# Kernel tuning notes

Hardware: AMD Instinct MI355X
Metric: run time of the kernel (lower is better)

Reference implementation:

```python
import jax, jax.numpy as jnp
import numpy as np

N_NODES = 100_000
N_EDGES_RAND = 800_000
N_GRAPHS = 2048
IN_FEATS = 74        # CanonicalAtomFeaturizer size
HEADS = 4            # dgllife GAT default num_heads
OUT_FEATS = 32       # dgllife GAT default hidden_feats=[32,32]
PRED_DIM = 128
NEG_SLOPE = 0.2      # dgllife default alpha


def setup_inputs() -> dict:
    key = jax.random.key(0)
    ks = jax.random.split(key, 16)
    feats = jax.random.normal(ks[0], (N_NODES, IN_FEATS), jnp.float32)
    src_r = jax.random.randint(ks[1], (N_EDGES_RAND,), 0, N_NODES, dtype=jnp.int32)
    dst_r = jax.random.randint(ks[2], (N_EDGES_RAND,), 0, N_NODES, dtype=jnp.int32)
    loops = jnp.arange(N_NODES, dtype=jnp.int32)  # self-loops -> no zero in-degree
    src = jnp.concatenate([src_r, loops])
    dst = jnp.concatenate([dst_r, loops])
    # sorted, every graph non-empty, ~49 nodes per molecule
    graph_ids = ((jnp.arange(N_NODES, dtype=jnp.int64) * N_GRAPHS) // N_NODES).astype(jnp.int32)

    def lin(k, i, o):
        return (jax.random.normal(k, (i, o), jnp.float32) / np.sqrt(i)).astype(jnp.float32)

    HF = HEADS * OUT_FEATS
    return {
        'feats': feats, 'src': src, 'dst': dst, 'graph_ids': graph_ids,
        'fc1_w': lin(ks[3], IN_FEATS, HF),
        'attn_l1': jax.random.normal(ks[4], (HEADS, OUT_FEATS), jnp.float32) * 0.1,
        'attn_r1': jax.random.normal(ks[5], (HEADS, OUT_FEATS), jnp.float32) * 0.1,
        'res1_w': lin(ks[6], IN_FEATS, HF),   # residual proj (in != heads*out)
        'bias1': jnp.zeros((HF,), jnp.float32),
        'fc2_w': lin(ks[7], HF, HF),
        'attn_l2': jax.random.normal(ks[8], (HEADS, OUT_FEATS), jnp.float32) * 0.1,
        'attn_r2': jax.random.normal(ks[9], (HEADS, OUT_FEATS), jnp.float32) * 0.1,
        'bias2': jnp.zeros((HF,), jnp.float32),
        'ww': lin(ks[10], OUT_FEATS, 1),
        'wb': jnp.zeros((1,), jnp.float32),
        'tw': lin(ks[11], 2 * OUT_FEATS, PRED_DIM),
        'tb': jnp.zeros((PRED_DIM,), jnp.float32),
    }


def _gat_conv(h, src, dst, fc_w, attn_l, attn_r, bias, res):
    # h: (N, Din) -> (N, H, F). Faithful to dgl.nn.GATConv (bias=True, residual=True).
    N = h.shape[0]
    feat = (h @ fc_w).reshape(N, HEADS, OUT_FEATS)          # (N,H,F)
    el = jnp.sum(feat * attn_l, axis=-1)                    # (N,H)
    er = jnp.sum(feat * attn_r, axis=-1)                    # (N,H)
    e = jax.nn.leaky_relu(el[src] + er[dst], NEG_SLOPE)     # (E,H)
    # edge softmax over incoming edges of each dst node (numerically stable)
    emax = jax.ops.segment_max(e, dst, num_segments=N)      # (N,H)
    ee = jnp.exp(e - emax[dst])
    denom = jax.ops.segment_sum(ee, dst, num_segments=N)    # (N,H)
    a = ee / denom[dst]                                     # (E,H)
    rst = jax.ops.segment_sum(a[:, :, None] * feat[src], dst, num_segments=N)  # (N,H,F)
    return rst + res + bias.reshape(1, HEADS, OUT_FEATS)


def reference(feats, src, dst, graph_ids, fc1_w, attn_l1, attn_r1, res1_w, bias1,
              fc2_w, attn_l2, attn_r2, bias2, ww, wb, tw, tb):
    N = feats.shape[0]
    # Layer 1: residual needs projection (74 != 128); agg 'flatten' + ELU
    res1 = (feats @ res1_w).reshape(N, HEADS, OUT_FEATS)
    h1 = _gat_conv(feats, src, dst, fc1_w, attn_l1, attn_r1, bias1, res1)
    h1 = jax.nn.elu(h1.reshape(N, HEADS * OUT_FEATS))
    # Layer 2: identity residual (128 == heads*out); agg 'mean', no activation
    res2 = h1.reshape(N, HEADS, OUT_FEATS)
    h2 = _gat_conv(h1, src, dst, fc2_w, attn_l2, attn_r2, bias2, res2)
    node_feats = jnp.mean(h2, axis=1)                       # (N, 32)
    # WeightedSumAndMax readout
    w = jax.nn.sigmoid(node_feats @ ww + wb)                # (N,1)
    h_sum = jax.ops.segment_sum(w * node_feats, graph_ids, num_segments=N_GRAPHS)
    h_max = jax.ops.segment_max(node_feats, graph_ids, num_segments=N_GRAPHS)
    g = jnp.concatenate([h_sum, h_max], axis=-1)            # (B, 64)
    return g @ tw + tb                                      # (B, PRED_DIM)
```

## Files before the change

kernel.cpp:

```cpp
#include <hip/hip_runtime.h>
#include <hip/hip_bf16.h>


#define HEADS 4
#define OUTF 32
#define HF 128
#define IN_FEATS 74
#define PRED_DIM 128
#define NEG_SLOPE 0.2f
#define NEG_INF_ENC 0x007fffffu
#define LOG2E 1.4426950408889634f
#define KP1 48
#define KP2 64

typedef __hip_bfloat16 bf16;
typedef __hip_bfloat162 bf16x2;
typedef __attribute__((ext_vector_type(8))) short bf16x8v;
typedef __attribute__((ext_vector_type(4))) float f32x4v;
typedef __attribute__((ext_vector_type(2))) float f32x2v;

__device__ __forceinline__ unsigned enc_f(float f) {
  unsigned u = __float_as_uint(f);
  return (u & 0x80000000u) ? ~u : (u | 0x80000000u);
}
__device__ __forceinline__ float dec_f(unsigned k) {
  return (k & 0x80000000u) ? __uint_as_float(k & 0x7fffffffu)
                           : __uint_as_float(~k);
}
__device__ __forceinline__ unsigned pack_bf16(float a, float b) {
  bf16x2 h = __float22bfloat162_rn(make_float2(a, b));
  return *(unsigned*)&h;
}
__device__ __forceinline__ float2 unpack_bf16(unsigned u) {
  bf16x2 h = *(bf16x2*)&u;
  return __bfloat1622float2(h);
}
__device__ __forceinline__ float lrelu(float v) {
  return fmaxf(v, NEG_SLOPE * v);
}

__global__ __launch_bounds__(256) void prep_w(
    const float* __restrict__ W1, const float* __restrict__ W2,
    const float* __restrict__ W3, unsigned* __restrict__ WT1,
    unsigned* __restrict__ WT2, unsigned* __restrict__ WT3,
    int* __restrict__ deg, int N) {
  int t = blockIdx.x * 256 + threadIdx.x;
  if (t < N) deg[t] = 0;
  if (t < 128 * KP1) {
    int c = t / KP1, kp = t % KP1;
    int k = kp * 2;
    float a1 = (k < IN_FEATS) ? W1[k * HF + c] : 0.f;
    float b1 = (k + 1 < IN_FEATS) ? W1[(k + 1) * HF + c] : 0.f;
    float a2 = (k < IN_FEATS) ? W2[k * HF + c] : 0.f;
    float b2 = (k + 1 < IN_FEATS) ? W2[(k + 1) * HF + c] : 0.f;
    WT1[t] = pack_bf16(a1, b1);
    WT2[t] = pack_bf16(a2, b2);
  } else {
    int u = t - 128 * KP1;
    if (u < 128 * KP2) {
      int c = u / KP2, kp = u % KP2;
      int k = kp * 2;
      WT3[u] = pack_bf16(W3[k * HF + c], W3[(k + 1) * HF + c]);
    }
  }
}


template <int K>
__device__ __forceinline__ bf16x8v load_a_f32(const float* __restrict__ X,
                                              int row, int N, int ks, int q) {
  unsigned v[4] = {0u, 0u, 0u, 0u};
  if (row < N) {
    const float* base = X + (size_t)row * K;
    int k = ks * 32 + q * 8;
#pragma unroll
    for (int j = 0; j < 4; ++j) {
      int kk = k + j * 2;
      if (kk + 1 < K) {
        float2 f = *(const float2*)&base[kk];
        v[j] = pack_bf16(f.x, f.y);
      } else if (kk < K) {
        v[j] = pack_bf16(base[kk], 0.f);
      }
    }
  }
  union { unsigned u[4]; bf16x8v v8; } r;
  r.u[0] = v[0]; r.u[1] = v[1]; r.u[2] = v[2]; r.u[3] = v[3];
  return r.v8;
}

__device__ __forceinline__ void scores_epilogue(
    const f32x4v* acc, const float* __restrict__ attn_l,
    const float* __restrict__ attn_r, float* __restrict__ el,
    float* __restrict__ er, int n0, int w, int q, int cc, int N) {
#pragma unroll
  for (int r = 0; r < 4; ++r) {
    int n = n0 + w * 16 + q * 4 + r;
    float pls[4], prs[4];
#pragma unroll
    for (int h = 0; h < 4; ++h) {
      float pl = acc[2 * h][r] * attn_l[h * 32 + cc] +
                 acc[2 * h + 1][r] * attn_l[h * 32 + 16 + cc];
      float pr = acc[2 * h][r] * attn_r[h * 32 + cc] +
                 acc[2 * h + 1][r] * attn_r[h * 32 + 16 + cc];
#pragma unroll
      for (int off = 1; off < 16; off <<= 1) {
        pl += __shfl_xor(pl, off);
        pr += __shfl_xor(pr, off);
      }
      pls[h] = pl;
      prs[h] = pr;
    }
    if (cc == 0 && n < N) {
#pragma unroll
      for (int h = 0; h < 4; ++h) {
        el[n * HEADS + h] = pls[h] * LOG2E;
        er[n * HEADS + h] = prs[h] * LOG2E;
      }
    }
  }
}

template <int K, int KP>
__global__ __launch_bounds__(256) void mfma_gemm(
    const bf16* __restrict__ X, const unsigned* __restrict__ WT,
    const float* __restrict__ attn_l, const float* __restrict__ attn_r,
    bf16* __restrict__ out, float* __restrict__ el, float* __restrict__ er,
    int N) {
  const int tid = threadIdx.x;
  const int w = tid >> 6;
  const int lane = tid & 63;
  const int cc = lane & 15;
  const int q = lane >> 4;
  const int n0 = blockIdx.x * 64;
  const int arow = n0 + w * 16 + cc;

  f32x4v acc[8];
#pragma unroll
  for (int t = 0; t < 8; ++t) acc[t] = f32x4v{0.f, 0.f, 0.f, 0.f};

  constexpr int KSTEPS = (K + 31) / 32;
#pragma unroll
  for (int ks = 0; ks < KSTEPS; ++ks) {
    bf16x8v a = *(const bf16x8v*)&X[(size_t)arow * K + ks * 32 + q * 8];
#pragma unroll
    for (int t = 0; t < 8; ++t) {
      bf16x8v b = *(const bf16x8v*)&WT[(t * 16 + cc) * KP + ks * 16 + q * 4];
      acc[t] = __builtin_amdgcn_mfma_f32_16x16x32_bf16(a, b, acc[t], 0, 0, 0);
    }
  }
#pragma unroll
  for (int r = 0; r < 4; ++r) {
    int n = n0 + w * 16 + q * 4 + r;
    if (n < N) {
#pragma unroll
      for (int t = 0; t < 8; ++t)
        out[(size_t)n * HF + t * 16 + cc] = __float2bfloat16(acc[t][r]);
    }
  }
  scores_epilogue(acc, attn_l, attn_r, el, er, n0, w, q, cc, N);
}

template <int K, int KP>
__global__ __launch_bounds__(256) void mfma_dual(
    const float* __restrict__ X, const unsigned* __restrict__ WT1,
    const unsigned* __restrict__ WT2, const float* __restrict__ attn_l,
    const float* __restrict__ attn_r, bf16* __restrict__ outA,
    bf16* __restrict__ outB, float* __restrict__ el, float* __restrict__ er,
    int N) {
  const int tid = threadIdx.x;
  const int w = tid >> 6;
  const int lane = tid & 63;
  const int cc = lane & 15;
  const int q = lane >> 4;
  const int n0 = blockIdx.x * 64;
  const int arow = n0 + w * 16 + cc;

  f32x4v acc1[8], acc2[8];
#pragma unroll
  for (int t = 0; t < 8; ++t) {
    acc1[t] = f32x4v{0.f, 0.f, 0.f, 0.f};
    acc2[t] = f32x4v{0.f, 0.f, 0.f, 0.f};
  }

  constexpr int KSTEPS = (K + 31) / 32;
#pragma unroll
  for (int ks = 0; ks < KSTEPS; ++ks) {
    bf16x8v a = load_a_f32<K>(X, arow, N, ks, q);
#pragma unroll
    for (int t = 0; t < 8; ++t) {
      bf16x8v b1 = *(const bf16x8v*)&WT1[(t * 16 + cc) * KP + ks * 16 + q * 4];
      bf16x8v b2 = *(const bf16x8v*)&WT2[(t * 16 + cc) * KP + ks * 16 + q * 4];
      acc1[t] = __builtin_amdgcn_mfma_f32_16x16x32_bf16(a, b1, acc1[t], 0, 0, 0);
      acc2[t] = __builtin_amdgcn_mfma_f32_16x16x32_bf16(a, b2, acc2[t], 0, 0, 0);
    }
  }
#pragma unroll
  for (int r = 0; r < 4; ++r) {
    int n = n0 + w * 16 + q * 4 + r;
    if (n < N) {
#pragma unroll
      for (int t = 0; t < 8; ++t) {
        outA[(size_t)n * HF + t * 16 + cc] = __float2bfloat16(acc1[t][r]);
        outB[(size_t)n * HF + t * 16 + cc] = __float2bfloat16(acc2[t][r]);
      }
    }
  }
  scores_epilogue(acc1, attn_l, attn_r, el, er, n0, w, q, cc, N);
}

__global__ __launch_bounds__(256) void hist_kernel(
    const int* __restrict__ dst, int* __restrict__ deg,
    int* __restrict__ rank, float* __restrict__ hsum,
    unsigned* __restrict__ hmax, int E, int g32) {
  int e = blockIdx.x * 256 + threadIdx.x;
  if (e < g32) {
    hsum[e] = 0.f;
    hmax[e] = NEG_INF_ENC;
  }
  if (e < E) rank[e] = atomicAdd(&deg[dst[e]], 1);
}

__global__ __launch_bounds__(256) void scan1_kernel(
    const int* __restrict__ deg, int* __restrict__ row_ptr,
    int* __restrict__ bsum, int N) {
  const int base = blockIdx.x * 2048;
  const int tbase = base + threadIdx.x * 8;
  int vals[8];
  int tsum = 0;
#pragma unroll
  for (int i = 0; i < 8; ++i) {
    int idx = tbase + i;
    vals[i] = (idx < N) ? deg[idx] : 0;
    tsum += vals[i];
  }
  const int lane = threadIdx.x & 63, wv = threadIdx.x >> 6;
  int incl = tsum;
#pragma unroll
  for (int off = 1; off < 64; off <<= 1) {
    int nv = __shfl_up(incl, off);
    if (lane >= off) incl += nv;
  }
  __shared__ int wsum[4];
  if (lane == 63) wsum[wv] = incl;
  __syncthreads();
  int woff = 0;
  for (int w = 0; w < wv; ++w) woff += wsum[w];
  int run = woff + incl - tsum;
#pragma unroll
  for (int i = 0; i < 8; ++i) {
    int idx = tbase + i;
    if (idx < N) row_ptr[idx] = run;
    run += vals[i];
  }
  if (threadIdx.x == 255) bsum[blockIdx.x] = woff + incl;
}

__global__ __launch_bounds__(64) void scan2_kernel(
    const int* __restrict__ bsum, int* __restrict__ bpre, int NB) {
  const int lane = threadIdx.x;
  int running = 0;
  for (int c = 0; c < NB; c += 64) {
    int v = (c + lane < NB) ? bsum[c + lane] : 0;
    int incl = v;
#pragma unroll
    for (int off = 1; off < 64; off <<= 1) {
      int nv = __shfl_up(incl, off);
      if (lane >= off) incl += nv;
    }
    if (c + lane < NB) bpre[c + lane] = running + incl - v;
    running += __shfl(incl, 63);
  }
}

__global__ __launch_bounds__(256) void scan3_kernel(
    int* __restrict__ row_ptr, const int* __restrict__ bpre, int N, int E) {
  int t = blockIdx.x * 256 + threadIdx.x;
  if (t < N) row_ptr[t] += bpre[t >> 11];
  if (t == 0) row_ptr[N] = E;
}

__global__ __launch_bounds__(256) void scatter_kernel(
    const int* __restrict__ src, const int* __restrict__ dst,
    const int* __restrict__ row_ptr, const int* __restrict__ rank,
    int* __restrict__ ssorted, int E) {
  int e = blockIdx.x * 256 + threadIdx.x;
  if (e >= E) return;
  if (e < 16) ssorted[E + e] = 0;
  int d = dst[e];
  ssorted[row_ptr[d] + rank[e]] = src[e];
}


#define E8_LOAD(i, e_)                                                      \
  const int s##i = __builtin_amdgcn_readfirstlane(ssorted[e_]);             \
  const float xl##i = el[(unsigned)s##i * HEADS + h];                       \
  const unsigned fu##i = *(const unsigned*)&feat[(unsigned)s##i * HF + c2];
#define E8_CALC(i)                                                          \
  {                                                                         \
    float xx = __builtin_amdgcn_exp2f(lrelu(xl##i + ern));                  \
    f32x2v ff;                                                              \
    ff.x = __uint_as_float(fu##i << 16);                                    \
    ff.y = __uint_as_float(fu##i & 0xffff0000u);                            \
    ssum += xx;                                                             \
    axy = __builtin_elementwise_fma(f32x2v{xx, xx}, ff, axy);               \
  }
#define E8_CALC_PRED(i, e_)                                                 \
  {                                                                         \
    float xx = __builtin_amdgcn_exp2f(lrelu(xl##i + ern));                  \
    xx = ((e_) + i < re) ? xx : 0.f;                                        \
    f32x2v ff;                                                              \
    ff.x = __uint_as_float(fu##i << 16);                                    \
    ff.y = __uint_as_float(fu##i & 0xffff0000u);                            \
    ssum += xx;                                                             \
    axy = __builtin_elementwise_fma(f32x2v{xx, xx}, ff, axy);               \
  }

#define AGG_LOOP                                                            \
  f32x2v axy = {0.f, 0.f};                                                  \
  float ssum = 0.f;                                                         \
  const int dg = re - rb;                                                   \
  if (dg <= 8) {                                                            \
    E8_LOAD(0, rb) E8_LOAD(1, rb + 1) E8_LOAD(2, rb + 2)                    \
    E8_LOAD(3, rb + 3) E8_LOAD(4, rb + 4) E8_LOAD(5, rb + 5)                \
    E8_LOAD(6, rb + 6) E8_LOAD(7, rb + 7)                                   \
    E8_CALC_PRED(0, rb) E8_CALC_PRED(1, rb) E8_CALC_PRED(2, rb)             \
    E8_CALC_PRED(3, rb) E8_CALC_PRED(4, rb) E8_CALC_PRED(5, rb)             \
    E8_CALC_PRED(6, rb) E8_CALC_PRED(7, rb)                                 \
  } else if (dg <= 16) {                                                    \
    E8_LOAD(0, rb) E8_LOAD(1, rb + 1) E8_LOAD(2, rb + 2)                    \
    E8_LOAD(3, rb + 3) E8_LOAD(4, rb + 4) E8_LOAD(5, rb + 5)                \
    E8_LOAD(6, rb + 6) E8_LOAD(7, rb + 7)                                   \
    E8_LOAD(8, rb + 8) E8_LOAD(9, rb + 9) E8_LOAD(10, rb + 10)              \
    E8_LOAD(11, rb + 11) E8_LOAD(12, rb + 12) E8_LOAD(13, rb + 13)          \
    E8_LOAD(14, rb + 14) E8_LOAD(15, rb + 15)                               \
    E8_CALC(0) E8_CALC(1) E8_CALC(2) E8_CALC(3)                             \
    E8_CALC(4) E8_CALC(5) E8_CALC(6) E8_CALC(7)                             \
    E8_CALC_PRED(8, rb) E8_CALC_PRED(9, rb) E8_CALC_PRED(10, rb)            \
    E8_CALC_PRED(11, rb) E8_CALC_PRED(12, rb) E8_CALC_PRED(13, rb)          \
    E8_CALC_PRED(14, rb) E8_CALC_PRED(15, rb)                               \
  } else {                                                                  \
    int e = rb;                                                             \
    for (; e + 8 <= re; e += 8) {                                           \
      E8_LOAD(0, e) E8_LOAD(1, e + 1) E8_LOAD(2, e + 2) E8_LOAD(3, e + 3)   \
      E8_LOAD(4, e + 4) E8_LOAD(5, e + 5) E8_LOAD(6, e + 6)                 \
      E8_LOAD(7, e + 7)                                                     \
      E8_CALC(0) E8_CALC(1) E8_CALC(2) E8_CALC(3)                           \
      E8_CALC(4) E8_CALC(5) E8_CALC(6) E8_CALC(7)                           \
    }                                                                       \
    if (e < re) {                                                           \
      E8_LOAD(0, e) E8_LOAD(1, e + 1) E8_LOAD(2, e + 2) E8_LOAD(3, e + 3)   \
      E8_LOAD(4, e + 4) E8_LOAD(5, e + 5) E8_LOAD(6, e + 6)                 \
      E8_LOAD(7, e + 7)                                                     \
      E8_CALC_PRED(0, e) E8_CALC_PRED(1, e) E8_CALC_PRED(2, e)              \
      E8_CALC_PRED(3, e) E8_CALC_PRED(4, e) E8_CALC_PRED(5, e)              \
      E8_CALC_PRED(6, e) E8_CALC_PRED(7, e)                                 \
    }                                                                       \
  }                                                                         \
  float ax = axy.x, ay = axy.y;

__global__ __launch_bounds__(256) void agg1_fused(
    const int* __restrict__ row_ptr, const int* __restrict__ ssorted,
    const float* __restrict__ el, const float* __restrict__ er,
    const bf16* __restrict__ feat, const bf16* __restrict__ res,
    bf16* __restrict__ H, const float* __restrict__ bias, int N) {
  int n = blockIdx.x * 4 + (threadIdx.x >> 6);
  if (n >= N) return;
  const int lane = threadIdx.x & 63;
  const int c2 = lane * 2, h = lane >> 4;
  const int rb = __builtin_amdgcn_readfirstlane(row_ptr[n]);
  const int re = __builtin_amdgcn_readfirstlane(row_ptr[n + 1]);
  const float ern = er[(unsigned)n * HEADS + h];

  AGG_LOOP

  float inv = 1.f / ssum;
  float2 r = unpack_bf16(*(const unsigned*)&res[(unsigned)n * HF + c2]);
  float2 bi = *(const float2*)&bias[c2];
  float vx = fmaf(ax, inv, r.x + bi.x);
  float vy = fmaf(ay, inv, r.y + bi.y);
  vx = (vx > 0.f) ? vx : expm1f(vx);
  vy = (vy > 0.f) ? vy : expm1f(vy);
  *(unsigned*)&H[(unsigned)n * HF + c2] = pack_bf16(vx, vy);
}

__global__ __launch_bounds__(256) void agg2_fused(
    const int* __restrict__ row_ptr, const int* __restrict__ ssorted,
    const float* __restrict__ el, const float* __restrict__ er,
    const bf16* __restrict__ feat, const bf16* __restrict__ h1,
    const float* __restrict__ bias, const float* __restrict__ ww,
    const float* __restrict__ wb, const int* __restrict__ gids,
    float* __restrict__ hsum, unsigned* __restrict__ hmax, int N) {
  int n = blockIdx.x * 4 + (threadIdx.x >> 6);
  if (n >= N) return;
  const int lane = threadIdx.x & 63;
  const int c2 = lane * 2, h = lane >> 4;
  const int rb = __builtin_amdgcn_readfirstlane(row_ptr[n]);
  const int re = __builtin_amdgcn_readfirstlane(row_ptr[n + 1]);
  const float ern = er[(unsigned)n * HEADS + h];

  AGG_LOOP

  float inv = 1.f / ssum;
  float2 r = unpack_bf16(*(const unsigned*)&h1[(unsigned)n * HF + c2]);
  float2 bi = *(const float2*)&bias[c2];
  ax = fmaf(ax, inv, r.x + bi.x);
  ay = fmaf(ay, inv, r.y + bi.y);
#pragma unroll
  for (int off = 16; off < 64; off <<= 1) {
    ax += __shfl_xor(ax, off);
    ay += __shfl_xor(ay, off);
  }
  ax *= 0.25f;
  ay *= 0.25f;
  int c = c2 & 31;
  float d = fmaf(ax, ww[c], ay * ww[c + 1]);
#pragma unroll
  for (int off = 1; off < 16; off <<= 1) d += __shfl_xor(d, off);
  float wv = 1.f / (1.f + __expf(-(d + wb[0])));
  if (lane < 16) {
    int g = gids[n];
    atomicAdd(&hsum[g * OUTF + c], wv * ax);
    atomicAdd(&hsum[g * OUTF + c + 1], wv * ay);
    atomicMax(&hmax[g * OUTF + c], enc_f(ax));
    atomicMax(&hmax[g * OUTF + c + 1], enc_f(ay));
  }
}

__global__ __launch_bounds__(256) void final_gemm_kernel(
    const float* __restrict__ hsum, const unsigned* __restrict__ hmax,
    const float* __restrict__ tw, const float* __restrict__ tb,
    float* __restrict__ out, int G) {
  __shared__ float tws[64 * PRED_DIM];
  for (int i = threadIdx.x; i < 64 * PRED_DIM; i += 256) tws[i] = tw[i];
  __syncthreads();
  int g = blockIdx.x * 2 + (threadIdx.x >> 7);
  int p = threadIdx.x & 127;
  if (g >= G) return;
  float acc = tb[p];
#pragma unroll
  for (int k = 0; k < OUTF; ++k)
    acc = fmaf(hsum[g * OUTF + k], tws[k * PRED_DIM + p], acc);
#pragma unroll
  for (int k = 0; k < OUTF; ++k)
    acc = fmaf(dec_f(hmax[g * OUTF + k]), tws[(OUTF + k) * PRED_DIM + p], acc);
  out[(size_t)g * PRED_DIM + p] = acc;
}

static inline int cdiv(long long a, int b) { return (int)((a + b - 1) / b); }

extern "C" void kernel_launch(void* const* d_in, const int* in_sizes, int n_in,
                              void* d_out, int out_size, void* d_ws,
                              size_t ws_size, hipStream_t stream) {
  const float* feats   = (const float*)d_in[0];
  const int*   src     = (const int*)d_in[1];
  const int*   dst     = (const int*)d_in[2];
  const int*   gids    = (const int*)d_in[3];
  const float* fc1_w   = (const float*)d_in[4];
  const float* attn_l1 = (const float*)d_in[5];
  const float* attn_r1 = (const float*)d_in[6];
  const float* res1_w  = (const float*)d_in[7];
  const float* bias1   = (const float*)d_in[8];
  const float* fc2_w   = (const float*)d_in[9];
  const float* attn_l2 = (const float*)d_in[10];
  const float* attn_r2 = (const float*)d_in[11];
  const float* bias2   = (const float*)d_in[12];
  const float* ww      = (const float*)d_in[13];
  const float* wb      = (const float*)d_in[14];
  const float* tw      = (const float*)d_in[15];
  const float* tb      = (const float*)d_in[16];
  float* out = (float*)d_out;

  const int N = in_sizes[0] / IN_FEATS;
  const int E = in_sizes[1];
  const int G = out_size / PRED_DIM;
  const int NB = cdiv(N, 2048);

  bf16* A = (bf16*)d_ws;
  bf16* B = A + (size_t)N * HF;
  bf16* H = B + (size_t)N * HF;
  float* el = (float*)(H + (size_t)N * HF);
  float* er = el + (size_t)N * HEADS;
  float* hsum = er + (size_t)N * HEADS;
  unsigned* hmax = (unsigned*)(hsum + (size_t)G * OUTF);
  int* deg     = (int*)(hmax + (size_t)G * OUTF);
  int* row_ptr = deg + N;
  int* ssorted = row_ptr + (N + 1);
  int* rank    = ssorted + E + 16;
  int* bsum    = rank + E;
  int* bpre    = bsum + NB;
  unsigned* WT1 = (unsigned*)(((uintptr_t)(bpre + NB) + 15) &
                              ~(uintptr_t)15);
  unsigned* WT2 = WT1 + 128 * KP1;
  unsigned* WT3 = WT2 + 128 * KP1;

  const int gblk = cdiv(N, 64);
  const int nwblk = cdiv(N, 4);

  prep_w<<<cdiv(N, 256), 256, 0, stream>>>(fc1_w, res1_w, fc2_w, WT1, WT2,
                                           WT3, deg, N);
  hist_kernel<<<cdiv(E, 256), 256, 0, stream>>>(dst, deg, rank, hsum, hmax, E,
                                                G * OUTF);
  scan1_kernel<<<NB, 256, 0, stream>>>(deg, row_ptr, bsum, N);
  scan2_kernel<<<1, 64, 0, stream>>>(bsum, bpre, NB);
  scan3_kernel<<<cdiv(N, 256), 256, 0, stream>>>(row_ptr, bpre, N, E);
  scatter_kernel<<<cdiv(E, 256), 256, 0, stream>>>(src, dst, row_ptr, rank,
                                                   ssorted, E);

  mfma_dual<IN_FEATS, KP1><<<gblk, 256, 0, stream>>>(
      feats, WT1, WT2, attn_l1, attn_r1, A, B, el, er, N);
  agg1_fused<<<nwblk, 256, 0, stream>>>(row_ptr, ssorted, el, er, A, B, H,
                                        bias1, N);

  mfma_gemm<HF, KP2><<<gblk, 256, 0, stream>>>(
      H, WT3, attn_l2, attn_r2, A, el, er, N);
  agg2_fused<<<nwblk, 256, 0, stream>>>(row_ptr, ssorted, el, er, A, H, bias2,
                                        ww, wb, gids, hsum, hmax, N);

  final_gemm_kernel<<<cdiv(G, 2), 256, 0, stream>>>(hsum, hmax, tw, tb, out, G);
}
```

Measured before the change: 350.0 us.

## Merge preprocessing kernels and use grid-stride aggregation to cut launches

Folds the weight-packing and degree-histogram kernels into one, moves the deg zeroing to a memset, fuses the two scan passes via a last-block ticket, and runs the edge scatter inside the layer-1 MFMA GEMM launch as extra blocks. The aggregation kernels become grid-stride loops over a fixed 2048-block grid. The aim is fewer kernel launches and less inter-kernel idle time in a short pipeline. The costs are a serial tail in the last scan block, a possible load-balance loss from the fixed grid, and reliance on the ticket counter being zeroed by the memset on every call.

```diff
diff --git a/kernel.cpp b/kernel.cpp
--- a/kernel.cpp
+++ b/kernel.cpp
@@ -39,13 +39,18 @@
   return fmaxf(v, NEG_SLOPE * v);
 }
 
-__global__ __launch_bounds__(256) void prep_w(
+__global__ __launch_bounds__(256) void hist_prep(
+    const int* __restrict__ dst, int* __restrict__ deg,
+    int* __restrict__ rank, float* __restrict__ hsum,
+    unsigned* __restrict__ hmax, int E, int g32,
     const float* __restrict__ W1, const float* __restrict__ W2,
     const float* __restrict__ W3, unsigned* __restrict__ WT1,
-    unsigned* __restrict__ WT2, unsigned* __restrict__ WT3,
-    int* __restrict__ deg, int N) {
+    unsigned* __restrict__ WT2, unsigned* __restrict__ WT3) {
   int t = blockIdx.x * 256 + threadIdx.x;
-  if (t < N) deg[t] = 0;
+  if (t < g32) {
+    hsum[t] = 0.f;
+    hmax[t] = NEG_INF_ENC;
+  }
   if (t < 128 * KP1) {
     int c = t / KP1, kp = t % KP1;
     int k = kp * 2;
@@ -55,14 +60,79 @@
     float b2 = (k + 1 < IN_FEATS) ? W2[(k + 1) * HF + c] : 0.f;
     WT1[t] = pack_bf16(a1, b1);
     WT2[t] = pack_bf16(a2, b2);
-  } else {
+  } else if (t - 128 * KP1 < 128 * KP2) {
     int u = t - 128 * KP1;
-    if (u < 128 * KP2) {
-      int c = u / KP2, kp = u % KP2;
-      int k = kp * 2;
-      WT3[u] = pack_bf16(W3[k * HF + c], W3[(k + 1) * HF + c]);
-    }
-  }
+    int c = u / KP2, kp = u % KP2;
+    int k = kp * 2;
+    WT3[u] = pack_bf16(W3[k * HF + c], W3[(k + 1) * HF + c]);
+  }
+  if (t < E) rank[t] = atomicAdd(&deg[dst[t]], 1);
+}
+
+__global__ __launch_bounds__(256) void scan12_kernel(
+    const int* __restrict__ deg, int* __restrict__ row_ptr,
+    int* __restrict__ bsum, int* __restrict__ bpre,
+    int* __restrict__ ticket, int N) {
+  const int base = blockIdx.x * 2048;
+  const int tbase = base + threadIdx.x * 8;
+  int vals[8];
+  int tsum = 0;
+#pragma unroll
+  for (int i = 0; i < 8; ++i) {
+    int idx = tbase + i;
+    vals[i] = (idx < N) ? deg[idx] : 0;
+    tsum += vals[i];
+  }
+  const int lane = threadIdx.x & 63, wv = threadIdx.x >> 6;
+  int incl = tsum;
+#pragma unroll
+  for (int off = 1; off < 64; off <<= 1) {
+    int nv = __shfl_up(incl, off);
+    if (lane >= off) incl += nv;
+  }
+  __shared__ int wsum[4];
+  __shared__ int isLast;
+  if (lane == 63) wsum[wv] = incl;
+  __syncthreads();
+  int woff = 0;
+  for (int w = 0; w < wv; ++w) woff += wsum[w];
+  int run = woff + incl - tsum;
+#pragma unroll
+  for (int i = 0; i < 8; ++i) {
+    int idx = tbase + i;
+    if (idx < N) row_ptr[idx] = run;
+    run += vals[i];
+  }
+  if (threadIdx.x == 255) {
+    bsum[blockIdx.x] = woff + incl;
+    __threadfence();
+    int t = atomicAdd(ticket, 1);
+    isLast = (t == (int)gridDim.x - 1);
+  }
+  __syncthreads();
+  if (isLast && threadIdx.x < 64) {
+    __threadfence();
+    const int NB = gridDim.x;
+    int running = 0;
+    for (int c = 0; c < NB; c += 64) {
+      int v = (c + lane < NB) ? bsum[c + lane] : 0;
+      int incl2 = v;
+#pragma unroll
+      for (int off = 1; off < 64; off <<= 1) {
+        int nv = __shfl_up(incl2, off);
+        if (lane >= off) incl2 += nv;
+      }
+      if (c + lane < NB) bpre[c + lane] = running + incl2 - v;
+      running += __shfl(incl2, 63);
+    }
+  }
+}
+
+__global__ __launch_bounds__(256) void scan3_kernel(
+    int* __restrict__ row_ptr, const int* __restrict__ bpre, int N, int E) {
+  int t = blockIdx.x * 256 + threadIdx.x;
+  if (t < N) row_ptr[t] += bpre[t >> 11];
+  if (t == 0) row_ptr[N] = E;
 }
 
 
@@ -161,19 +231,29 @@
   scores_epilogue(acc, attn_l, attn_r, el, er, n0, w, q, cc, N);
 }
 
-template <int K, int KP>
-__global__ __launch_bounds__(256) void mfma_dual(
+__global__ __launch_bounds__(256) void scat_mfma1(
+    const int* __restrict__ src, const int* __restrict__ dst,
+    const int* __restrict__ row_ptr, const int* __restrict__ rank,
+    int* __restrict__ ssorted, int E, int SB,
     const float* __restrict__ X, const unsigned* __restrict__ WT1,
     const unsigned* __restrict__ WT2, const float* __restrict__ attn_l,
     const float* __restrict__ attn_r, bf16* __restrict__ outA,
     bf16* __restrict__ outB, float* __restrict__ el, float* __restrict__ er,
     int N) {
+  if ((int)blockIdx.x < SB) {
+    int e = blockIdx.x * 256 + threadIdx.x;
+    if (e >= E) return;
+    if (e < 16) ssorted[E + e] = 0;
+    int d = dst[e];
+    ssorted[row_ptr[d] + rank[e]] = src[e];
+    return;
+  }
   const int tid = threadIdx.x;
   const int w = tid >> 6;
   const int lane = tid & 63;
   const int cc = lane & 15;
   const int q = lane >> 4;
-  const int n0 = blockIdx.x * 64;
+  const int n0 = ((int)blockIdx.x - SB) * 64;
   const int arow = n0 + w * 16 + cc;
 
   f32x4v acc1[8], acc2[8];
@@ -183,14 +263,14 @@
     acc2[t] = f32x4v{0.f, 0.f, 0.f, 0.f};
   }
 
-  constexpr int KSTEPS = (K + 31) / 32;
+  constexpr int KSTEPS = (IN_FEATS + 31) / 32;
 #pragma unroll
   for (int ks = 0; ks < KSTEPS; ++ks) {
-    bf16x8v a = load_a_f32<K>(X, arow, N, ks, q);
+    bf16x8v a = load_a_f32<IN_FEATS>(X, arow, N, ks, q);
 #pragma unroll
     for (int t = 0; t < 8; ++t) {
-      bf16x8v b1 = *(const bf16x8v*)&WT1[(t * 16 + cc) * KP + ks * 16 + q * 4];
-      bf16x8v b2 = *(const bf16x8v*)&WT2[(t * 16 + cc) * KP + ks * 16 + q * 4];
+      bf16x8v b1 = *(const bf16x8v*)&WT1[(t * 16 + cc) * KP1 + ks * 16 + q * 4];
+      bf16x8v b2 = *(const bf16x8v*)&WT2[(t * 16 + cc) * KP1 + ks * 16 + q * 4];
       acc1[t] = __builtin_amdgcn_mfma_f32_16x16x32_bf16(a, b1, acc1[t], 0, 0, 0);
       acc2[t] = __builtin_amdgcn_mfma_f32_16x16x32_bf16(a, b2, acc2[t], 0, 0, 0);
     }
@@ -207,88 +287,6 @@
     }
   }
   scores_epilogue(acc1, attn_l, attn_r, el, er, n0, w, q, cc, N);
-}
-
-__global__ __launch_bounds__(256) void hist_kernel(
-    const int* __restrict__ dst, int* __restrict__ deg,
-    int* __restrict__ rank, float* __restrict__ hsum,
-    unsigned* __restrict__ hmax, int E, int g32) {
-  int e = blockIdx.x * 256 + threadIdx.x;
-  if (e < g32) {
-    hsum[e] = 0.f;
-    hmax[e] = NEG_INF_ENC;
-  }
-  if (e < E) rank[e] = atomicAdd(&deg[dst[e]], 1);
-}
-
-__global__ __launch_bounds__(256) void scan1_kernel(
-    const int* __restrict__ deg, int* __restrict__ row_ptr,
-    int* __restrict__ bsum, int N) {
-  const int base = blockIdx.x * 2048;
-  const int tbase = base + threadIdx.x * 8;
-  int vals[8];
-  int tsum = 0;
-#pragma unroll
-  for (int i = 0; i < 8; ++i) {
-    int idx = tbase + i;
-    vals[i] = (idx < N) ? deg[idx] : 0;
-    tsum += vals[i];
-  }
-  const int lane = threadIdx.x & 63, wv = threadIdx.x >> 6;
-  int incl = tsum;
-#pragma unroll
-  for (int off = 1; off < 64; off <<= 1) {
-    int nv = __shfl_up(incl, off);
-    if (lane >= off) incl += nv;
-  }
-  __shared__ int wsum[4];
-  if (lane == 63) wsum[wv] = incl;
-  __syncthreads();
-  int woff = 0;
-  for (int w = 0; w < wv; ++w) woff += wsum[w];
-  int run = woff + incl - tsum;
-#pragma unroll
-  for (int i = 0; i < 8; ++i) {
-    int idx = tbase + i;
-    if (idx < N) row_ptr[idx] = run;
-    run += vals[i];
-  }
-  if (threadIdx.x == 255) bsum[blockIdx.x] = woff + incl;
-}
-
-__global__ __launch_bounds__(64) void scan2_kernel(
-    const int* __restrict__ bsum, int* __restrict__ bpre, int NB) {
-  const int lane = threadIdx.x;
-  int running = 0;
-  for (int c = 0; c < NB; c += 64) {
-    int v = (c + lane < NB) ? bsum[c + lane] : 0;
-    int incl = v;
-#pragma unroll
-    for (int off = 1; off < 64; off <<= 1) {
-      int nv = __shfl_up(incl, off);
-      if (lane >= off) incl += nv;
-    }
-    if (c + lane < NB) bpre[c + lane] = running + incl - v;
-    running += __shfl(incl, 63);
-  }
-}
-
-__global__ __launch_bounds__(256) void scan3_kernel(
-    int* __restrict__ row_ptr, const int* __restrict__ bpre, int N, int E) {
-  int t = blockIdx.x * 256 + threadIdx.x;
-  if (t < N) row_ptr[t] += bpre[t >> 11];
-  if (t == 0) row_ptr[N] = E;
-}
-
-__global__ __launch_bounds__(256) void scatter_kernel(
-    const int* __restrict__ src, const int* __restrict__ dst,
-    const int* __restrict__ row_ptr, const int* __restrict__ rank,
-    int* __restrict__ ssorted, int E) {
-  int e = blockIdx.x * 256 + threadIdx.x;
-  if (e >= E) return;
-  if (e < 16) ssorted[E + e] = 0;
-  int d = dst[e];
-  ssorted[row_ptr[d] + rank[e]] = src[e];
 }
 
 
@@ -364,24 +362,26 @@
     const float* __restrict__ el, const float* __restrict__ er,
     const bf16* __restrict__ feat, const bf16* __restrict__ res,
     bf16* __restrict__ H, const float* __restrict__ bias, int N) {
-  int n = blockIdx.x * 4 + (threadIdx.x >> 6);
-  if (n >= N) return;
   const int lane = threadIdx.x & 63;
   const int c2 = lane * 2, h = lane >> 4;
-  const int rb = __builtin_amdgcn_readfirstlane(row_ptr[n]);
-  const int re = __builtin_amdgcn_readfirstlane(row_ptr[n + 1]);
-  const float ern = er[(unsigned)n * HEADS + h];
-
-  AGG_LOOP
-
-  float inv = 1.f / ssum;
-  float2 r = unpack_bf16(*(const unsigned*)&res[(unsigned)n * HF + c2]);
-  float2 bi = *(const float2*)&bias[c2];
-  float vx = fmaf(ax, inv, r.x + bi.x);
-  float vy = fmaf(ay, inv, r.y + bi.y);
-  vx = (vx > 0.f) ? vx : expm1f(vx);
-  vy = (vy > 0.f) ? vy : expm1f(vy);
-  *(unsigned*)&H[(unsigned)n * HF + c2] = pack_bf16(vx, vy);
+  const int wl = threadIdx.x >> 6;
+  for (int nb = blockIdx.x; nb * 4 + wl < N; nb += gridDim.x) {
+    const int n = nb * 4 + wl;
+    const int rb = __builtin_amdgcn_readfirstlane(row_ptr[n]);
+    const int re = __builtin_amdgcn_readfirstlane(row_ptr[n + 1]);
+    const float ern = er[(unsigned)n * HEADS + h];
+
+    AGG_LOOP
+
+    float inv = 1.f / ssum;
+    float2 r = unpack_bf16(*(const unsigned*)&res[(unsigned)n * HF + c2]);
+    float2 bi = *(const float2*)&bias[c2];
+    float vx = fmaf(ax, inv, r.x + bi.x);
+    float vy = fmaf(ay, inv, r.y + bi.y);
+    vx = (vx > 0.f) ? vx : expm1f(vx);
+    vy = (vy > 0.f) ? vy : expm1f(vy);
+    *(unsigned*)&H[(unsigned)n * HF + c2] = pack_bf16(vx, vy);
+  }
 }
 
 __global__ __launch_bounds__(256) void agg2_fused(
@@ -391,39 +391,41 @@
     const float* __restrict__ bias, const float* __restrict__ ww,
     const float* __restrict__ wb, const int* __restrict__ gids,
     float* __restrict__ hsum, unsigned* __restrict__ hmax, int N) {
-  int n = blockIdx.x * 4 + (threadIdx.x >> 6);
-  if (n >= N) return;
   const int lane = threadIdx.x & 63;
   const int c2 = lane * 2, h = lane >> 4;
-  const int rb = __builtin_amdgcn_readfirstlane(row_ptr[n]);
-  const int re = __builtin_amdgcn_readfirstlane(row_ptr[n + 1]);
-  const float ern = er[(unsigned)n * HEADS + h];
-
-  AGG_LOOP
-
-  float inv = 1.f / ssum;
-  float2 r = unpack_bf16(*(const unsigned*)&h1[(unsigned)n * HF + c2]);
-  float2 bi = *(const float2*)&bias[c2];
-  ax = fmaf(ax, inv, r.x + bi.x);
-  ay = fmaf(ay, inv, r.y + bi.y);
-#pragma unroll
-  for (int off = 16; off < 64; off <<= 1) {
-    ax += __shfl_xor(ax, off);
-    ay += __shfl_xor(ay, off);
-  }
-  ax *= 0.25f;
-  ay *= 0.25f;
-  int c = c2 & 31;
-  float d = fmaf(ax, ww[c], ay * ww[c + 1]);
-#pragma unroll
-  for (int off = 1; off < 16; off <<= 1) d += __shfl_xor(d, off);
-  float wv = 1.f / (1.f + __expf(-(d + wb[0])));
-  if (lane < 16) {
-    int g = gids[n];
-    atomicAdd(&hsum[g * OUTF + c], wv * ax);
-    atomicAdd(&hsum[g * OUTF + c + 1], wv * ay);
-    atomicMax(&hmax[g * OUTF + c], enc_f(ax));
-    atomicMax(&hmax[g * OUTF + c + 1], enc_f(ay));
+  const int wl = threadIdx.x >> 6;
+  for (int nb = blockIdx.x; nb * 4 + wl < N; nb += gridDim.x) {
+    const int n = nb * 4 + wl;
+    const int rb = __builtin_amdgcn_readfirstlane(row_ptr[n]);
+    const int re = __builtin_amdgcn_readfirstlane(row_ptr[n + 1]);
+    const float ern = er[(unsigned)n * HEADS + h];
+
+    AGG_LOOP
+
+    float inv = 1.f / ssum;
+    float2 r = unpack_bf16(*(const unsigned*)&h1[(unsigned)n * HF + c2]);
+    float2 bi = *(const float2*)&bias[c2];
+    ax = fmaf(ax, inv, r.x + bi.x);
+    ay = fmaf(ay, inv, r.y + bi.y);
+#pragma unroll
+    for (int off = 16; off < 64; off <<= 1) {
+      ax += __shfl_xor(ax, off);
+      ay += __shfl_xor(ay, off);
+    }
+    ax *= 0.25f;
+    ay *= 0.25f;
+    int c = c2 & 31;
+    float d = fmaf(ax, ww[c], ay * ww[c + 1]);
+#pragma unroll
+    for (int off = 1; off < 16; off <<= 1) d += __shfl_xor(d, off);
+    float wv = 1.f / (1.f + __expf(-(d + wb[0])));
+    if (lane < 16) {
+      int g = gids[n];
+      atomicAdd(&hsum[g * OUTF + c], wv * ax);
+      atomicAdd(&hsum[g * OUTF + c + 1], wv * ay);
+      atomicMax(&hmax[g * OUTF + c], enc_f(ax));
+      atomicMax(&hmax[g * OUTF + c + 1], enc_f(ay));
+    }
   }
 }
 
@@ -484,7 +486,8 @@
   float* hsum = er + (size_t)N * HEADS;
   unsigned* hmax = (unsigned*)(hsum + (size_t)G * OUTF);
   int* deg     = (int*)(hmax + (size_t)G * OUTF);
-  int* row_ptr = deg + N;
+  int* ticket  = deg + N;
+  int* row_ptr = deg + N + 1;
   int* ssorted = row_ptr + (N + 1);
   int* rank    = ssorted + E + 16;
   int* bsum    = rank + E;
@@ -495,27 +498,24 @@
   unsigned* WT3 = WT2 + 128 * KP1;
 
   const int gblk = cdiv(N, 64);
-  const int nwblk = cdiv(N, 4);
-
-  prep_w<<<cdiv(N, 256), 256, 0, stream>>>(fc1_w, res1_w, fc2_w, WT1, WT2,
-                                           WT3, deg, N);
-  hist_kernel<<<cdiv(E, 256), 256, 0, stream>>>(dst, deg, rank, hsum, hmax, E,
-                                                G * OUTF);
-  scan1_kernel<<<NB, 256, 0, stream>>>(deg, row_ptr, bsum, N);
-  scan2_kernel<<<1, 64, 0, stream>>>(bsum, bpre, NB);
+  const int SB = cdiv(E, 256);
+
+  hipMemsetAsync(deg, 0, (size_t)(N + 1) * sizeof(int), stream);
+  hist_prep<<<SB, 256, 0, stream>>>(dst, deg, rank, hsum, hmax, E, G * OUTF,
+                                    fc1_w, res1_w, fc2_w, WT1, WT2, WT3);
+  scan12_kernel<<<NB, 256, 0, stream>>>(deg, row_ptr, bsum, bpre, ticket, N);
   scan3_kernel<<<cdiv(N, 256), 256, 0, stream>>>(row_ptr, bpre, N, E);
-  scatter_kernel<<<cdiv(E, 256), 256, 0, stream>>>(src, dst, row_ptr, rank,
-                                                   ssorted, E);
-
-  mfma_dual<IN_FEATS, KP1><<<gblk, 256, 0, stream>>>(
-      feats, WT1, WT2, attn_l1, attn_r1, A, B, el, er, N);
-  agg1_fused<<<nwblk, 256, 0, stream>>>(row_ptr, ssorted, el, er, A, B, H,
-                                        bias1, N);
+
+  scat_mfma1<<<SB + gblk, 256, 0, stream>>>(
+      src, dst, row_ptr, rank, ssorted, E, SB, feats, WT1, WT2, attn_l1,
+      attn_r1, A, B, el, er, N);
+  agg1_fused<<<2048, 256, 0, stream>>>(row_ptr, ssorted, el, er, A, B, H,
+                                       bias1, N);
 
   mfma_gemm<HF, KP2><<<gblk, 256, 0, stream>>>(
       H, WT3, attn_l2, attn_r2, A, el, er, N);
-  agg2_fused<<<nwblk, 256, 0, stream>>>(row_ptr, ssorted, el, er, A, H, bias2,
-                                        ww, wb, gids, hsum, hmax, N);
+  agg2_fused<<<2048, 256, 0, stream>>>(row_ptr, ssorted, el, er, A, H, bias2,
+                                       ww, wb, gids, hsum, hmax, N);
 
   final_gemm_kernel<<<cdiv(G, 2), 256, 0, stream>>>(hsum, hmax, tw, tb, out, G);
 }
```

Measured after the change: 361.3 us. 3.2% more time.
